# Optimization experiments

Measured on AMD Instinct MI355X. Metric: run time of the kernel, lower is better.

## Reference

```python
import jax, jax.numpy as jnp
import numpy as np


def setup_inputs() -> dict:
    key = jax.random.key(0)
    k1, k2 = jax.random.split(key)
    N, D, G = 1000000, 128, 4096
    x = jax.random.normal(k1, (N, D), dtype=jnp.float32)
    batch = jnp.sort(jax.random.randint(k2, (N,), 0, G, dtype=jnp.int64))
    return {"x": x, "batch": batch, "num_graphs": G}


def reference(x, batch, num_graphs):
    # Single-pass segment max: [num_nodes, D] -> [num_graphs, D]
    # (equivalent to torch per-graph masked max, but O(N) scatter-reduce)
    return jax.ops.segment_max(x, batch, num_segments=num_graphs)
```

## Files before the change

kernel.cpp:

```cpp
#include <hip/hip_runtime.h>

typedef float float4v __attribute__((ext_vector_type(4)));

#define DIM 128

__global__ __launch_bounds__(256) void find_starts_kernel(
    const int* __restrict__ batch, int* __restrict__ starts, int N, int G)
{
    int i = blockIdx.x * blockDim.x + threadIdx.x;
    if (i >= N) return;
    int b = batch[i];
    int prev = (i == 0) ? -1 : batch[i - 1];
    for (int g = prev + 1; g <= b; ++g) starts[g] = i;
    if (i == N - 1) {
        for (int g = b + 1; g <= G; ++g) starts[g] = N;
    }
}

__global__ __launch_bounds__(256) void segmax_direct_kernel(
    const float* __restrict__ x, const int* __restrict__ starts,
    float* __restrict__ out, int G)
{
    int gtid = blockIdx.x * blockDim.x + threadIdx.x;
    int seg = gtid >> 6;
    int lane = threadIdx.x & 63;
    if (seg >= G) return;

    int r0 = starts[seg];
    int r1 = starts[seg + 1];

    int half = lane >> 5;
    int c = (lane & 31) * 4;

    float4v acc;
    acc.x = -INFINITY; acc.y = -INFINITY; acc.z = -INFINITY; acc.w = -INFINITY;

    const float* xc = x + c;
    int r = r0 + half;

    for (; r + 6 < r1; r += 8) {
        float4v v0 = *(const float4v*)(xc + (size_t)r * DIM);
        float4v v1 = *(const float4v*)(xc + (size_t)(r + 2) * DIM);
        float4v v2 = *(const float4v*)(xc + (size_t)(r + 4) * DIM);
        float4v v3 = *(const float4v*)(xc + (size_t)(r + 6) * DIM);
        acc.x = fmaxf(fmaxf(acc.x, v0.x), fmaxf(v1.x, v2.x));
        acc.y = fmaxf(fmaxf(acc.y, v0.y), fmaxf(v1.y, v2.y));
        acc.z = fmaxf(fmaxf(acc.z, v0.z), fmaxf(v1.z, v2.z));
        acc.w = fmaxf(fmaxf(acc.w, v0.w), fmaxf(v1.w, v2.w));
        acc.x = fmaxf(acc.x, v3.x);
        acc.y = fmaxf(acc.y, v3.y);
        acc.z = fmaxf(acc.z, v3.z);
        acc.w = fmaxf(acc.w, v3.w);
    }
    for (; r < r1; r += 2) {
        float4v v = *(const float4v*)(xc + (size_t)r * DIM);
        acc.x = fmaxf(acc.x, v.x);
        acc.y = fmaxf(acc.y, v.y);
        acc.z = fmaxf(acc.z, v.z);
        acc.w = fmaxf(acc.w, v.w);
    }

    acc.x = fmaxf(acc.x, __shfl_xor(acc.x, 32));
    acc.y = fmaxf(acc.y, __shfl_xor(acc.y, 32));
    acc.z = fmaxf(acc.z, __shfl_xor(acc.z, 32));
    acc.w = fmaxf(acc.w, __shfl_xor(acc.w, 32));

    if (half == 0) {
        *(float4v*)(out + (size_t)seg * DIM + c) = acc;
    }
}

extern "C" void kernel_launch(void* const* d_in, const int* in_sizes, int n_in,
                              void* d_out, int out_size, void* d_ws, size_t ws_size,
                              hipStream_t stream) {
    const float* x = (const float*)d_in[0];
    const int* batch = (const int*)d_in[1];
    float* out = (float*)d_out;

    int N = in_sizes[1];
    int G = out_size / DIM;

    int* starts = (int*)d_ws;

    {
        int threads = 256;
        int blocks = (N + threads - 1) / threads;
        find_starts_kernel<<<blocks, threads, 0, stream>>>(batch, starts, N, G);
    }

    {
        int waves = G;
        int blocks = (waves * 64 + 255) / 256;
        segmax_direct_kernel<<<blocks, 256, 0, stream>>>(x, starts, out, G);
    }
}
```

Baseline: 100.5 us.

## Fuse segment-start search into max kernel and use one block per segment

Drops the separate find_starts kernel: each block now binary-searches the sorted batch array to find its segment's row range, which removes one launch and the workspace round trip. Each segment is handled by four waves instead of one, with rows interleaved across waves and a shared-memory reduction at the end. This raises parallelism per segment, since each segment has about 244 rows, in exchange for redundant log-N binary searches per wave, a __syncthreads, and a larger grid.

```diff
diff --git a/kernel.cpp b/kernel.cpp
--- a/kernel.cpp
+++ b/kernel.cpp
@@ -4,45 +4,39 @@
 
 #define DIM 128
 
-__global__ __launch_bounds__(256) void find_starts_kernel(
-    const int* __restrict__ batch, int* __restrict__ starts, int N, int G)
+__global__ __launch_bounds__(256, 8) void segmax_block_kernel(
+    const float* __restrict__ x, const int* __restrict__ batch,
+    float* __restrict__ out, int N)
 {
-    int i = blockIdx.x * blockDim.x + threadIdx.x;
-    if (i >= N) return;
-    int b = batch[i];
-    int prev = (i == 0) ? -1 : batch[i - 1];
-    for (int g = prev + 1; g <= b; ++g) starts[g] = i;
-    if (i == N - 1) {
-        for (int g = b + 1; g <= G; ++g) starts[g] = N;
-    }
-}
+    __shared__ float red[4][DIM];
 
-__global__ __launch_bounds__(256) void segmax_direct_kernel(
-    const float* __restrict__ x, const int* __restrict__ starts,
-    float* __restrict__ out, int G)
-{
-    int gtid = blockIdx.x * blockDim.x + threadIdx.x;
-    int seg = gtid >> 6;
-    int lane = threadIdx.x & 63;
-    if (seg >= G) return;
-
-    int r0 = starts[seg];
-    int r1 = starts[seg + 1];
-
+    int seg = blockIdx.x;
+    int tid = threadIdx.x;
+    int w = tid >> 6;
+    int lane = tid & 63;
     int half = lane >> 5;
     int c = (lane & 31) * 4;
+
+    int g = seg + (lane & 1);
+    int lo = 0, hi = N;
+    while (lo < hi) {
+        int mid = (lo + hi) >> 1;
+        if (batch[mid] < g) lo = mid + 1; else hi = mid;
+    }
+    int r0 = __shfl(lo, 0);
+    int r1 = __shfl(lo, 1);
 
     float4v acc;
     acc.x = -INFINITY; acc.y = -INFINITY; acc.z = -INFINITY; acc.w = -INFINITY;
 
     const float* xc = x + c;
-    int r = r0 + half;
+    int r = r0 + 2 * w + half;
 
-    for (; r + 6 < r1; r += 8) {
+    for (; r + 24 < r1; r += 32) {
         float4v v0 = *(const float4v*)(xc + (size_t)r * DIM);
-        float4v v1 = *(const float4v*)(xc + (size_t)(r + 2) * DIM);
-        float4v v2 = *(const float4v*)(xc + (size_t)(r + 4) * DIM);
-        float4v v3 = *(const float4v*)(xc + (size_t)(r + 6) * DIM);
+        float4v v1 = *(const float4v*)(xc + (size_t)(r + 8) * DIM);
+        float4v v2 = *(const float4v*)(xc + (size_t)(r + 16) * DIM);
+        float4v v3 = *(const float4v*)(xc + (size_t)(r + 24) * DIM);
         acc.x = fmaxf(fmaxf(acc.x, v0.x), fmaxf(v1.x, v2.x));
         acc.y = fmaxf(fmaxf(acc.y, v0.y), fmaxf(v1.y, v2.y));
         acc.z = fmaxf(fmaxf(acc.z, v0.z), fmaxf(v1.z, v2.z));
@@ -52,7 +46,7 @@
         acc.z = fmaxf(acc.z, v3.z);
         acc.w = fmaxf(acc.w, v3.w);
     }
-    for (; r < r1; r += 2) {
+    for (; r < r1; r += 8) {
         float4v v = *(const float4v*)(xc + (size_t)r * DIM);
         acc.x = fmaxf(acc.x, v.x);
         acc.y = fmaxf(acc.y, v.y);
@@ -66,7 +60,20 @@
     acc.w = fmaxf(acc.w, __shfl_xor(acc.w, 32));
 
     if (half == 0) {
-        *(float4v*)(out + (size_t)seg * DIM + c) = acc;
+        *(float4v*)&red[w][c] = acc;
+    }
+    __syncthreads();
+    if (tid < 32) {
+        int cc = tid * 4;
+        float4v a = *(const float4v*)&red[0][cc];
+        float4v b = *(const float4v*)&red[1][cc];
+        float4v d = *(const float4v*)&red[2][cc];
+        float4v e = *(const float4v*)&red[3][cc];
+        a.x = fmaxf(fmaxf(a.x, b.x), fmaxf(d.x, e.x));
+        a.y = fmaxf(fmaxf(a.y, b.y), fmaxf(d.y, e.y));
+        a.z = fmaxf(fmaxf(a.z, b.z), fmaxf(d.z, e.z));
+        a.w = fmaxf(fmaxf(a.w, b.w), fmaxf(d.w, e.w));
+        *(float4v*)(out + (size_t)seg * DIM + cc) = a;
     }
 }
 
@@ -80,17 +87,5 @@
     int N = in_sizes[1];
     int G = out_size / DIM;
 
-    int* starts = (int*)d_ws;
-
-    {
-        int threads = 256;
-        int blocks = (N + threads - 1) / threads;
-        find_starts_kernel<<<blocks, threads, 0, stream>>>(batch, starts, N, G);
-    }
-
-    {
-        int waves = G;
-        int blocks = (waves * 64 + 255) / 256;
-        segmax_direct_kernel<<<blocks, 256, 0, stream>>>(x, starts, out, G);
-    }
+    segmax_block_kernel<<<G, 256, 0, stream>>>(x, batch, out, N);
 }
```

Result: slower. 102.9 us (+2.4%).
